# Performance work log

Hardware: AMD Instinct MI355X
Metric: run time of the kernel (lower is better)

The kernel has to match this reference:

```python
import jax, jax.numpy as jnp
import numpy as np

B, S, C, H = 8, 1024, 512, 8
DH = C // H  # channels per head


def setup_inputs() -> dict:
    key = jax.random.key(0)
    ks = jax.random.split(key, 10)
    s = 1.0 / np.sqrt(C)
    return {
        "pe_lin_encoding": jax.random.normal(ks[0], (B, S, C), jnp.float32),
        "pe_lin_skip": jax.random.normal(ks[1], (B, S, C), jnp.float32),
        "Wq": jax.random.normal(ks[2], (C, C), jnp.float32) * s,
        "bq": jax.random.normal(ks[3], (C,), jnp.float32) * s,
        "Wk": jax.random.normal(ks[4], (C, C), jnp.float32) * s,
        "bk": jax.random.normal(ks[5], (C,), jnp.float32) * s,
        "Wv": jax.random.normal(ks[6], (C, C), jnp.float32) * s,
        "bv": jax.random.normal(ks[7], (C,), jnp.float32) * s,
        "Wo": jax.random.normal(ks[8], (C, C), jnp.float32) * s,
        "bo": jax.random.normal(ks[9], (C,), jnp.float32) * s,
    }


def reference(pe_lin_encoding, pe_lin_skip, Wq, bq, Wk, bk, Wv, bv, Wo, bo):
    # flatten trailing dims (already [B, S, C] here)
    x = pe_lin_encoding.reshape(pe_lin_encoding.shape[0], pe_lin_encoding.shape[1], -1)
    # torch Linear convention: y = x @ W^T + b, W is [out, in]
    q = jnp.einsum("bsc,oc->bso", x, Wq) + bq
    k = jnp.einsum("bsc,oc->bso", x, Wk) + bk
    v = jnp.einsum("bsc,oc->bso", x, Wv) + bv
    # split heads: [B, S, H, DH] -> attention per head
    q = q.reshape(B, S, H, DH)
    k = k.reshape(B, S, H, DH)
    v = v.reshape(B, S, H, DH)
    scale = 1.0 / np.sqrt(DH)
    scores = jnp.einsum("bqhd,bkhd->bhqk", q, k) * scale  # [B,H,S,S]
    attn = jax.nn.softmax(scores, axis=-1)
    ctx = jnp.einsum("bhqk,bkhd->bqhd", attn, v).reshape(B, S, C)
    out = jnp.einsum("bsc,oc->bso", ctx, Wo) + bo
    return out + pe_lin_skip
```

## Files before the change

kernel.cpp:

```cpp
#include <hip/hip_runtime.h>
#include <hip/hip_bf16.h>

typedef unsigned short u16;
typedef unsigned int u32;

constexpr int B  = 8;
constexpr int S  = 1024;
constexpr int C  = 512;
constexpr int H  = 8;
constexpr int DH = 64;
constexpr int M  = B * S;

typedef __attribute__((ext_vector_type(8))) short bf16x8;
typedef __attribute__((ext_vector_type(4))) float f32x4;

#define GLOBAL_AS __attribute__((address_space(1)))
#define LDS_AS    __attribute__((address_space(3)))

#define QSCALE 0.1803368867f

__device__ __forceinline__ float bf2f(u16 u) {
    return __uint_as_float(((u32)u) << 16);
}
__device__ __forceinline__ u16 f2bf(float f) {
    u32 u = __float_as_uint(f);
    u += 0x7fffu + ((u >> 16) & 1u);
    return (u16)(u >> 16);
}
__device__ __forceinline__ u32 pack2(float a, float b) {
    return (u32)f2bf(a) | ((u32)f2bf(b) << 16);
}
__device__ __forceinline__ void async_cp16(const u16* g, u16* l) {
    __builtin_amdgcn_global_load_lds((const GLOBAL_AS void*)g, (LDS_AS void*)l, 16, 0, 0);
}

constexpr int NX4 = M * C / 4;
constexpr int NW4 = C * C / 4;

__global__ __launch_bounds__(256) void cvt_kernel(
    const float* __restrict__ x,
    const float* __restrict__ wq, const float* __restrict__ wk,
    const float* __restrict__ wv, const float* __restrict__ wo,
    u16* __restrict__ xb, u16* __restrict__ wqkv, u16* __restrict__ wob)
{
    const int i = blockIdx.x * 256 + threadIdx.x;
    const float* src; u16* dst; int off;
    if      (i < NX4)          { src = x;  dst = xb;           off = i; }
    else if (i < NX4 +   NW4)  { src = wq; dst = wqkv;         off = i - NX4; }
    else if (i < NX4 + 2*NW4)  { src = wk; dst = wqkv + C*C;   off = i - NX4 -   NW4; }
    else if (i < NX4 + 3*NW4)  { src = wv; dst = wqkv + 2*C*C; off = i - NX4 - 2*NW4; }
    else                       { src = wo; dst = wob;          off = i - NX4 - 3*NW4; }
    float4 v = ((const float4*)src)[off];
    uint2 p; p.x = pack2(v.x, v.y); p.y = pack2(v.z, v.w);
    ((uint2*)dst)[off] = p;
}

__global__ __launch_bounds__(256) void qkv_gemm(
    const u16* __restrict__ xb, const u16* __restrict__ wqkv,
    const float* __restrict__ bq, const float* __restrict__ bk,
    const float* __restrict__ bv,
    u16* __restrict__ Qo, u16* __restrict__ Ko, u16* __restrict__ Vo)
{
    __shared__ alignas(16) u16 smem[128 * 136];
    u16* const Asm = smem;
    u16* const Bsm = smem + 128 * 64;

    const int mTile = blockIdx.x * 128;
    const int nTile = blockIdx.y * 128;
    const int t = threadIdx.x, lane = t & 63, w = t >> 6;
    const int ql = lane & 15, quad = lane >> 4;
    const int wm = (w & 1) * 64, wn = (w >> 1) * 64;

    f32x4 acc[4][4];
    #pragma unroll
    for (int i = 0; i < 4; i++)
        #pragma unroll
        for (int j = 0; j < 4; j++) acc[i][j] = (f32x4){0.f, 0.f, 0.f, 0.f};

    for (int k0 = 0; k0 < C; k0 += 64) {
        __syncthreads();
        #pragma unroll
        for (int q = 0; q < 4; q++) {
            const int chunk = q * 256 + t;
            const int row = chunk >> 3, c8 = (chunk & 7) * 8;
            async_cp16(xb   + (size_t)(mTile + row) * C + k0 + c8, &Asm[row * 64 + c8]);
            async_cp16(wqkv + (size_t)(nTile + row) * C + k0 + c8, &Bsm[row * 64 + c8]);
        }
        __syncthreads();

        #pragma unroll
        for (int ks = 0; ks < 64; ks += 32) {
            bf16x8 af[4], bfr[4];
            #pragma unroll
            for (int i = 0; i < 4; i++)
                af[i] = *(const bf16x8*)&Asm[(wm + i*16 + ql) * 64 + ks + quad*8];
            #pragma unroll
            for (int j = 0; j < 4; j++)
                bfr[j] = *(const bf16x8*)&Bsm[(wn + j*16 + ql) * 64 + ks + quad*8];
            #pragma unroll
            for (int i = 0; i < 4; i++)
                #pragma unroll
                for (int j = 0; j < 4; j++)
                    acc[i][j] = __builtin_amdgcn_mfma_f32_16x16x32_bf16(af[i], bfr[j], acc[i][j], 0, 0, 0);
        }
    }

    const int z = nTile >> 9;
    const int nBase = nTile & 511;
    const float* bias = (z == 0) ? bq : (z == 1) ? bk : bv;
    const float sc    = (z == 0) ? QSCALE : 1.0f;

    __syncthreads();
    u16* const T = smem;
    #pragma unroll
    for (int j = 0; j < 4; j++) {
        const int n = wn + j*16 + ql;
        const float bj = bias[nBase + n];
        #pragma unroll
        for (int i = 0; i < 4; i++) {
            #pragma unroll
            for (int r = 0; r < 4; r++) {
                const int m = wm + i*16 + quad*4 + r;
                const u16 val = f2bf((acc[i][j][r] + bj) * sc);
                if (z == 2) T[n * 136 + m] = val;
                else        T[m * 136 + n] = val;
            }
        }
    }
    __syncthreads();

    if (z == 2) {
        const int bb = mTile >> 10, ssBase = mTile & 1023;
        #pragma unroll
        for (int q = 0; q < 8; q++) {
            const int c = q * 256 + t;
            const int row = c >> 4, col = (c & 15) * 8;
            const int o = nBase + row, h = o >> 6, d = o & 63;
            *(float4*)(Vo + ((size_t)((bb*H + h) * DH + d)) * S + ssBase + col) =
                *(const float4*)&T[row * 136 + col];
        }
    } else {
        u16* dst = (z == 0) ? Qo : Ko;
        #pragma unroll
        for (int q = 0; q < 8; q++) {
            const int c = q * 256 + t;
            const int row = c >> 4, col = (c & 15) * 8;
            *(float4*)(dst + (size_t)(mTile + row) * C + nBase + col) =
                *(const float4*)&T[row * 136 + col];
        }
    }
}

__global__ __launch_bounds__(512) void attn_kernel(
    const u16* __restrict__ Qo,
    const u16* __restrict__ Ko,
    const u16* __restrict__ Vo,
    u16* __restrict__ ctx)
{
    __shared__ alignas(16) u16 KsU[64 * 64];
    __shared__ alignas(16) u16 VsU[64 * 64];
    __shared__ alignas(16) u16 Ps [128 * 72];

    const int g = blockIdx.x;
    const int xcd = g & 7, slot = g >> 3;
    const int bh = xcd * 8 + (slot >> 3);
    const int qt = slot & 7;
    const int b_ = bh >> 3, h = bh & 7;

    const int t = threadIdx.x;
    const int lane = t & 63, w = t >> 6;
    const int ql = lane & 15, quad = lane >> 4;

    const u16* Qb = Qo + (size_t)b_ * S * C + h * DH;
    const u16* Kb = Ko + (size_t)b_ * S * C + h * DH;
    const u16* Vt = Vo + (size_t)bh * DH * S;

    const int qrow = qt*128 + w*16 + ql;
    const bf16x8 qf0 = *(const bf16x8*)(Qb + (size_t)qrow * C + quad*8);
    const bf16x8 qf1 = *(const bf16x8*)(Qb + (size_t)qrow * C + 32 + quad*8);

    bf16x8 onesf;
    #pragma unroll
    for (int i = 0; i < 8; i++) onesf[i] = (short)0x3F80;

    const int swzA = ((quad       ^ (ql & 7)) << 3);
    const int swzB = (((quad + 4) ^ (ql & 7)) << 3);

    const int srow = t >> 3, scc = t & 7;
    const int sgc8 = ((scc ^ (srow & 7)) << 3);

    f32x4 acc[4], accl;
    #pragma unroll
    for (int dt = 0; dt < 4; dt++) acc[dt] = (f32x4){0.f, 0.f, 0.f, 0.f};
    accl = (f32x4){0.f, 0.f, 0.f, 0.f};

    for (int k0 = 0; k0 < S; k0 += 64) {
        __syncthreads();
        async_cp16(Kb + (size_t)(k0 + srow) * C + sgc8, &KsU[t * 8]);
        async_cp16(Vt + (size_t)srow * S + k0 + sgc8,   &VsU[t * 8]);
        __syncthreads();

        f32x4 sc[4];
        #pragma unroll
        for (int nt = 0; nt < 4; nt++) {
            sc[nt] = (f32x4){0.f, 0.f, 0.f, 0.f};
            const bf16x8 kf0 = *(const bf16x8*)&KsU[(nt*16 + ql) * 64 + swzA];
            const bf16x8 kf1 = *(const bf16x8*)&KsU[(nt*16 + ql) * 64 + swzB];
            sc[nt] = __builtin_amdgcn_mfma_f32_16x16x32_bf16(qf0, kf0, sc[nt], 0, 0, 0);
            sc[nt] = __builtin_amdgcn_mfma_f32_16x16x32_bf16(qf1, kf1, sc[nt], 0, 0, 0);
        }

        #pragma unroll
        for (int r = 0; r < 4; r++) {
            const int prow = w*16 + quad*4 + r;
            Ps[prow * 72 +  0 + ql] = f2bf(exp2f(sc[0][r]));
            Ps[prow * 72 + 16 + ql] = f2bf(exp2f(sc[1][r]));
            Ps[prow * 72 + 32 + ql] = f2bf(exp2f(sc[2][r]));
            Ps[prow * 72 + 48 + ql] = f2bf(exp2f(sc[3][r]));
        }

        #pragma unroll
        for (int c = 0; c < 2; c++) {
            const bf16x8 pf = *(const bf16x8*)&Ps[(w*16 + ql) * 72 + c*32 + quad*8];
            const int swz = (c == 0) ? swzA : swzB;
            #pragma unroll
            for (int dt = 0; dt < 4; dt++) {
                const bf16x8 vf = *(const bf16x8*)&VsU[(dt*16 + ql) * 64 + swz];
                acc[dt] = __builtin_amdgcn_mfma_f32_16x16x32_bf16(pf, vf, acc[dt], 0, 0, 0);
            }
            accl = __builtin_amdgcn_mfma_f32_16x16x32_bf16(pf, onesf, accl, 0, 0, 0);
        }
    }

    #pragma unroll
    for (int r = 0; r < 4; r++) {
        const float inv = 1.0f / accl[r];
        const int orow = qt*128 + w*16 + quad*4 + r;
        const size_t base = ((size_t)(b_*S + orow)) * C + h*DH;
        #pragma unroll
        for (int dt = 0; dt < 4; dt++)
            ctx[base + dt*16 + ql] = f2bf(acc[dt][r] * inv);
    }
}

__global__ __launch_bounds__(256) void out_gemm(
    const u16* __restrict__ ctx, const u16* __restrict__ wob,
    const float* __restrict__ bo, const float* __restrict__ skip,
    float* __restrict__ out)
{
    __shared__ alignas(16) u16 Asm[128 * 64];
    __shared__ alignas(16) u16 Bsm[128 * 64];

    const int mTile = blockIdx.x * 128;
    const int nTile = blockIdx.y * 128;
    const int t = threadIdx.x, lane = t & 63, w = t >> 6;
    const int ql = lane & 15, quad = lane >> 4;
    const int wm = (w & 1) * 64, wn = (w >> 1) * 64;

    f32x4 acc[4][4];
    #pragma unroll
    for (int i = 0; i < 4; i++)
        #pragma unroll
        for (int j = 0; j < 4; j++) acc[i][j] = (f32x4){0.f, 0.f, 0.f, 0.f};

    for (int k0 = 0; k0 < C; k0 += 64) {
        __syncthreads();
        #pragma unroll
        for (int q = 0; q < 4; q++) {
            const int chunk = q * 256 + t;
            const int row = chunk >> 3, c8 = (chunk & 7) * 8;
            async_cp16(ctx + (size_t)(mTile + row) * C + k0 + c8, &Asm[row * 64 + c8]);
            async_cp16(wob + (size_t)(nTile + row) * C + k0 + c8, &Bsm[row * 64 + c8]);
        }
        __syncthreads();

        #pragma unroll
        for (int ks = 0; ks < 64; ks += 32) {
            bf16x8 af[4], bfr[4];
            #pragma unroll
            for (int i = 0; i < 4; i++)
                af[i] = *(const bf16x8*)&Asm[(wm + i*16 + ql) * 64 + ks + quad*8];
            #pragma unroll
            for (int j = 0; j < 4; j++)
                bfr[j] = *(const bf16x8*)&Bsm[(wn + j*16 + ql) * 64 + ks + quad*8];
            #pragma unroll
            for (int i = 0; i < 4; i++)
                #pragma unroll
                for (int j = 0; j < 4; j++)
                    acc[i][j] = __builtin_amdgcn_mfma_f32_16x16x32_bf16(af[i], bfr[j], acc[i][j], 0, 0, 0);
        }
    }

    #pragma unroll
    for (int j = 0; j < 4; j++) {
        const int o = nTile + wn + j*16 + ql;
        const float bj = bo[o];
        #pragma unroll
        for (int i = 0; i < 4; i++) {
            #pragma unroll
            for (int r = 0; r < 4; r++) {
                const int m = mTile + wm + i*16 + quad*4 + r;
                const size_t idx = (size_t)m * C + o;
                out[idx] = acc[i][j][r] + bj + skip[idx];
            }
        }
    }
}

extern "C" void kernel_launch(void* const* d_in, const int* in_sizes, int n_in,
                              void* d_out, int out_size, void* d_ws, size_t ws_size,
                              hipStream_t stream) {
    (void)in_sizes; (void)n_in; (void)out_size; (void)ws_size;
    const float* x    = (const float*)d_in[0];
    const float* skip = (const float*)d_in[1];
    const float* Wq   = (const float*)d_in[2];
    const float* bq   = (const float*)d_in[3];
    const float* Wk   = (const float*)d_in[4];
    const float* bk   = (const float*)d_in[5];
    const float* Wv   = (const float*)d_in[6];
    const float* bv   = (const float*)d_in[7];
    const float* Wo   = (const float*)d_in[8];
    const float* bo   = (const float*)d_in[9];
    float* out = (float*)d_out;

    u16* xb   = (u16*)d_ws;
    u16* wqkv = xb   + (size_t)M * C;
    u16* wob  = wqkv + (size_t)3 * C * C;
    u16* Qo   = wob  + (size_t)C * C;
    u16* Ko   = Qo   + (size_t)M * C;
    u16* Vo   = Ko   + (size_t)M * C;
    u16* ctx  = xb;

    cvt_kernel<<<dim3((NX4 + 4 * NW4) / 256), 256, 0, stream>>>(
        x, Wq, Wk, Wv, Wo, xb, wqkv, wob);
    qkv_gemm<<<dim3(M / 128, 1536 / 128), 256, 0, stream>>>(
        xb, wqkv, bq, bk, bv, Qo, Ko, Vo);
    attn_kernel<<<dim3(512), 512, 0, stream>>>(Qo, Ko, Vo, ctx);
    out_gemm<<<dim3(M / 128, C / 128), 256, 0, stream>>>(
        ctx, wob, bo, skip, out);
}
```

Before: 177.6 us.

## Fuse fp32-to-bf16 conversion into GEMM tile loads and shrink out_gemm M tile

Removes the separate conversion kernel and instead converts fp32 inputs and weights to bf16 while staging tiles into LDS inside the QKV and output GEMMs. This avoids a full pass writing and re-reading bf16 copies of x and the weights, plus one launch. The output GEMM M tile is halved to 64 to double the block count. In exchange, the GEMMs read fp32 data (twice the bytes) repeatedly across N tiles, and the synchronous load-convert-store replaces asynchronous global-to-LDS copies.

```diff
diff --git a/kernel.cpp b/kernel.cpp
--- a/kernel.cpp
+++ b/kernel.cpp
@@ -19,44 +19,33 @@
 
 #define QSCALE 0.1803368867f
 
-__device__ __forceinline__ float bf2f(u16 u) {
-    return __uint_as_float(((u32)u) << 16);
-}
 __device__ __forceinline__ u16 f2bf(float f) {
     u32 u = __float_as_uint(f);
     u += 0x7fffu + ((u >> 16) & 1u);
     return (u16)(u >> 16);
 }
-__device__ __forceinline__ u32 pack2(float a, float b) {
-    return (u32)f2bf(a) | ((u32)f2bf(b) << 16);
-}
 __device__ __forceinline__ void async_cp16(const u16* g, u16* l) {
     __builtin_amdgcn_global_load_lds((const GLOBAL_AS void*)g, (LDS_AS void*)l, 16, 0, 0);
 }
-
-constexpr int NX4 = M * C / 4;
-constexpr int NW4 = C * C / 4;
-
-__global__ __launch_bounds__(256) void cvt_kernel(
+__device__ __forceinline__ void cvt_store8(u16* lds, const float* g) {
+    const float4 a = *(const float4*)g;
+    const float4 b = *(const float4*)(g + 4);
+    __hip_bfloat162 p0 = __float22bfloat162_rn(make_float2(a.x, a.y));
+    __hip_bfloat162 p1 = __float22bfloat162_rn(make_float2(a.z, a.w));
+    __hip_bfloat162 p2 = __float22bfloat162_rn(make_float2(b.x, b.y));
+    __hip_bfloat162 p3 = __float22bfloat162_rn(make_float2(b.z, b.w));
+    uint4 o;
+    o.x = *reinterpret_cast<u32*>(&p0);
+    o.y = *reinterpret_cast<u32*>(&p1);
+    o.z = *reinterpret_cast<u32*>(&p2);
+    o.w = *reinterpret_cast<u32*>(&p3);
+    *(uint4*)lds = o;
+}
+
+__global__ __launch_bounds__(256) void qkv_gemm(
     const float* __restrict__ x,
     const float* __restrict__ wq, const float* __restrict__ wk,
-    const float* __restrict__ wv, const float* __restrict__ wo,
-    u16* __restrict__ xb, u16* __restrict__ wqkv, u16* __restrict__ wob)
-{
-    const int i = blockIdx.x * 256 + threadIdx.x;
-    const float* src; u16* dst; int off;
-    if      (i < NX4)          { src = x;  dst = xb;           off = i; }
-    else if (i < NX4 +   NW4)  { src = wq; dst = wqkv;         off = i - NX4; }
-    else if (i < NX4 + 2*NW4)  { src = wk; dst = wqkv + C*C;   off = i - NX4 -   NW4; }
-    else if (i < NX4 + 3*NW4)  { src = wv; dst = wqkv + 2*C*C; off = i - NX4 - 2*NW4; }
-    else                       { src = wo; dst = wob;          off = i - NX4 - 3*NW4; }
-    float4 v = ((const float4*)src)[off];
-    uint2 p; p.x = pack2(v.x, v.y); p.y = pack2(v.z, v.w);
-    ((uint2*)dst)[off] = p;
-}
-
-__global__ __launch_bounds__(256) void qkv_gemm(
-    const u16* __restrict__ xb, const u16* __restrict__ wqkv,
+    const float* __restrict__ wv,
     const float* __restrict__ bq, const float* __restrict__ bk,
     const float* __restrict__ bv,
     u16* __restrict__ Qo, u16* __restrict__ Ko, u16* __restrict__ Vo)
@@ -71,6 +60,10 @@
     const int ql = lane & 15, quad = lane >> 4;
     const int wm = (w & 1) * 64, wn = (w >> 1) * 64;
 
+    const int z = nTile >> 9;
+    const int nBase = nTile & 511;
+    const float* Wsrc = (z == 0) ? wq : (z == 1) ? wk : wv;
+
     f32x4 acc[4][4];
     #pragma unroll
     for (int i = 0; i < 4; i++)
@@ -83,8 +76,8 @@
         for (int q = 0; q < 4; q++) {
             const int chunk = q * 256 + t;
             const int row = chunk >> 3, c8 = (chunk & 7) * 8;
-            async_cp16(xb   + (size_t)(mTile + row) * C + k0 + c8, &Asm[row * 64 + c8]);
-            async_cp16(wqkv + (size_t)(nTile + row) * C + k0 + c8, &Bsm[row * 64 + c8]);
+            cvt_store8(&Asm[chunk * 8], x    + (size_t)(mTile + row) * C + k0 + c8);
+            cvt_store8(&Bsm[chunk * 8], Wsrc + (size_t)(nBase + row) * C + k0 + c8);
         }
         __syncthreads();
 
@@ -105,8 +98,6 @@
         }
     }
 
-    const int z = nTile >> 9;
-    const int nBase = nTile & 511;
     const float* bias = (z == 0) ? bq : (z == 1) ? bk : bv;
     const float sc    = (z == 0) ? QSCALE : 1.0f;
 
@@ -244,47 +235,52 @@
 }
 
 __global__ __launch_bounds__(256) void out_gemm(
-    const u16* __restrict__ ctx, const u16* __restrict__ wob,
+    const u16* __restrict__ ctx, const float* __restrict__ wo,
     const float* __restrict__ bo, const float* __restrict__ skip,
     float* __restrict__ out)
 {
-    __shared__ alignas(16) u16 Asm[128 * 64];
-    __shared__ alignas(16) u16 Bsm[128 * 64];
-
-    const int mTile = blockIdx.x * 128;
+    __shared__ alignas(16) u16 Ab[64 * 64];
+    __shared__ alignas(16) u16 Bb[128 * 64];
+
+    const int mTile = blockIdx.x * 64;
     const int nTile = blockIdx.y * 128;
     const int t = threadIdx.x, lane = t & 63, w = t >> 6;
     const int ql = lane & 15, quad = lane >> 4;
-    const int wm = (w & 1) * 64, wn = (w >> 1) * 64;
-
-    f32x4 acc[4][4];
-    #pragma unroll
-    for (int i = 0; i < 4; i++)
+    const int wm = (w & 1) * 32, wn = (w >> 1) * 64;
+
+    f32x4 acc[2][4];
+    #pragma unroll
+    for (int i = 0; i < 2; i++)
         #pragma unroll
         for (int j = 0; j < 4; j++) acc[i][j] = (f32x4){0.f, 0.f, 0.f, 0.f};
 
     for (int k0 = 0; k0 < C; k0 += 64) {
         __syncthreads();
+        #pragma unroll
+        for (int q = 0; q < 2; q++) {
+            const int chunk = q * 256 + t;
+            const int row = chunk >> 3, c8 = (chunk & 7) * 8;
+            async_cp16(ctx + (size_t)(mTile + row) * C + k0 + c8, &Ab[chunk * 8]);
+        }
         #pragma unroll
         for (int q = 0; q < 4; q++) {
             const int chunk = q * 256 + t;
             const int row = chunk >> 3, c8 = (chunk & 7) * 8;
-            async_cp16(ctx + (size_t)(mTile + row) * C + k0 + c8, &Asm[row * 64 + c8]);
-            async_cp16(wob + (size_t)(nTile + row) * C + k0 + c8, &Bsm[row * 64 + c8]);
+            cvt_store8(&Bb[chunk * 8], wo + (size_t)(nTile + row) * C + k0 + c8);
         }
         __syncthreads();
 
         #pragma unroll
         for (int ks = 0; ks < 64; ks += 32) {
-            bf16x8 af[4], bfr[4];
-            #pragma unroll
-            for (int i = 0; i < 4; i++)
-                af[i] = *(const bf16x8*)&Asm[(wm + i*16 + ql) * 64 + ks + quad*8];
+            bf16x8 af[2], bfr[4];
+            #pragma unroll
+            for (int i = 0; i < 2; i++)
+                af[i] = *(const bf16x8*)&Ab[(wm + i*16 + ql) * 64 + ks + quad*8];
             #pragma unroll
             for (int j = 0; j < 4; j++)
-                bfr[j] = *(const bf16x8*)&Bsm[(wn + j*16 + ql) * 64 + ks + quad*8];
-            #pragma unroll
-            for (int i = 0; i < 4; i++)
+                bfr[j] = *(const bf16x8*)&Bb[(wn + j*16 + ql) * 64 + ks + quad*8];
+            #pragma unroll
+            for (int i = 0; i < 2; i++)
                 #pragma unroll
                 for (int j = 0; j < 4; j++)
                     acc[i][j] = __builtin_amdgcn_mfma_f32_16x16x32_bf16(af[i], bfr[j], acc[i][j], 0, 0, 0);
@@ -296,7 +292,7 @@
         const int o = nTile + wn + j*16 + ql;
         const float bj = bo[o];
         #pragma unroll
-        for (int i = 0; i < 4; i++) {
+        for (int i = 0; i < 2; i++) {
             #pragma unroll
             for (int r = 0; r < 4; r++) {
                 const int m = mTile + wm + i*16 + quad*4 + r;
@@ -323,19 +319,14 @@
     const float* bo   = (const float*)d_in[9];
     float* out = (float*)d_out;
 
-    u16* xb   = (u16*)d_ws;
-    u16* wqkv = xb   + (size_t)M * C;
-    u16* wob  = wqkv + (size_t)3 * C * C;
-    u16* Qo   = wob  + (size_t)C * C;
-    u16* Ko   = Qo   + (size_t)M * C;
-    u16* Vo   = Ko   + (size_t)M * C;
-    u16* ctx  = xb;
-
-    cvt_kernel<<<dim3((NX4 + 4 * NW4) / 256), 256, 0, stream>>>(
-        x, Wq, Wk, Wv, Wo, xb, wqkv, wob);
+    u16* Qo  = (u16*)d_ws;
+    u16* Ko  = Qo  + (size_t)M * C;
+    u16* Vo  = Ko  + (size_t)M * C;
+    u16* ctx = Vo  + (size_t)M * C;
+
     qkv_gemm<<<dim3(M / 128, 1536 / 128), 256, 0, stream>>>(
-        xb, wqkv, bq, bk, bv, Qo, Ko, Vo);
+        x, Wq, Wk, Wv, bq, bk, bv, Qo, Ko, Vo);
     attn_kernel<<<dim3(512), 512, 0, stream>>>(Qo, Ko, Vo, ctx);
-    out_gemm<<<dim3(M / 128, C / 128), 256, 0, stream>>>(
-        ctx, wob, bo, skip, out);
-}
+    out_gemm<<<dim3(M / 64, C / 128), 256, 0, stream>>>(
+        ctx, Wo, bo, skip, out);
+}
```

Measured after the change: 179.5 us. About the same (+1.1%).
